# Kernel tuning notes

Measured on AMD Instinct MI355X. Metric: run time of the kernel, lower is better.

Reference implementation:

```python
import jax, jax.numpy as jnp
import numpy as np

C_IN, C_OUT, K, H, W = 16, 16, 3, 1024, 1024
PAD = 1  # 'same' padding for 3x3 stride-1


def setup_inputs() -> dict:
    key = jax.random.key(0)
    kx, kw, kb = jax.random.split(key, 3)
    x = jax.random.normal(kx, (1, C_IN, H, W), dtype=jnp.float32)
    weight = jax.random.normal(kw, (C_OUT, C_IN, K, K), dtype=jnp.float32) * 0.05
    bias = jax.random.normal(kb, (C_OUT,), dtype=jnp.float32) * 0.05
    return {"x": x, "weight": weight, "bias": bias}


def reference(x, weight, bias):
    # Original module: im2col (unfold) + matmul + reshape + bias add.
    # Mathematically identical to a dense 2D convolution (cross-correlation),
    # expressed here as the fused implicit-GEMM conv primitive.
    out = jax.lax.conv_general_dilated(
        x, weight,
        window_strides=(1, 1),
        padding=((PAD, PAD), (PAD, PAD)),
        dimension_numbers=("NCHW", "OIHW", "NCHW"),
    )  # [1, C_OUT, H, W]
    # out_unf.view(*output_shape) drops the batch dim (batch must be 1)
    return out[0] + bias[:, None, None]
```

## Files before the change

kernel.cpp:

```cpp
#include <hip/hip_runtime.h>


#define HH 1024
#define WW 1024
#define CIN 16
#define COUT 16
#define TW 64
#define TH 16
#define LROWS (TH + 2)
#define LCOLS (TW + 2)
#define PIX 16
#define NPIX (LROWS * LCOLS)

typedef short v8s __attribute__((ext_vector_type(8)));
typedef float v4f __attribute__((ext_vector_type(4)));
typedef unsigned int u32;

__device__ __forceinline__ unsigned short f32_bf16(float f) {
    union { float f; u32 u; } v;
    v.f = f;
    u32 u = v.u;
    u += 0x7fffu + ((u >> 16) & 1u);
    return (unsigned short)(u >> 16);
}

__device__ __forceinline__ int swz(int c) { return c ^ ((c >> 3) & 7); }

__global__ __launch_bounds__(256, 3)
void conv3x3_fused(const float* __restrict__ x,
                   const float* __restrict__ wgt,
                   const float* __restrict__ bias,
                   float* __restrict__ out) {
    __shared__ __align__(16) unsigned short sm[NPIX * PIX];
    __shared__ __align__(16) unsigned short wsm[20 * 16 * 8];

    const int tid = threadIdx.x;
    const int lane = tid & 63;
    const int wave = tid >> 6;
    const int h0 = blockIdx.y * TH;
    const int w0 = blockIdx.x * TW;

    if (tid < 32) ((uint4*)(wsm + 18 * 16 * 8))[tid] = make_uint4(0u, 0u, 0u, 0u);
    #pragma unroll
    for (int s = 0; s < 9; ++s) {
        const int e = s * 256 + tid;
        const int m = e / 144;
        const int rem = e - m * 144;
        const int c = rem / 9;
        const int r9 = rem - c * 9;
        const int t = r9 * 2 + (c >> 3);
        wsm[(t * 16 + m) * 8 + (c & 7)] = f32_bf16(wgt[e]);
    }

    auto stage_body = [&](int b) {
        const int r = b >> 4;
        const int j = b & 15;
        const int gh = h0 - 1 + r;
        const int pbase = r * LCOLS + 1 + 4 * j;
        float4 f4[CIN];
        if ((unsigned)gh < (unsigned)HH) {
            const float4* src = (const float4*)(x + (size_t)gh * WW + w0) + j;
            #pragma unroll
            for (int c = 0; c < CIN; ++c)
                f4[c] = src[(size_t)c * (HH * WW / 4)];
        } else {
            #pragma unroll
            for (int c = 0; c < CIN; ++c)
                f4[c] = make_float4(0.f, 0.f, 0.f, 0.f);
        }
        #pragma unroll
        for (int k = 0; k < 4; ++k) {
            u32 pk[8];
            #pragma unroll
            for (int i = 0; i < 8; ++i) {
                const float lo = ((const float*)&f4[2 * i])[k];
                const float hi = ((const float*)&f4[2 * i + 1])[k];
                pk[i] = (u32)f32_bf16(lo) | ((u32)f32_bf16(hi) << 16);
            }
            #pragma unroll
            for (int half = 0; half < 2; ++half) {
                const int cc = 2 * pbase + 2 * k + half;
                *(uint4*)(sm + swz(cc) * 8) = *(uint4*)&pk[half * 4];
            }
        }
    };
    auto stage_halo = [&](int h) {
        const int r = h >> 1;
        const int side = h & 1;
        const int gh = h0 - 1 + r;
        const int gw = side ? (w0 + 64) : (w0 - 1);
        const int p = r * LCOLS + (side ? 65 : 0);
        float f[CIN];
        if ((unsigned)gh < (unsigned)HH && (unsigned)gw < (unsigned)WW) {
            const float* src = x + (size_t)gh * WW + gw;
            #pragma unroll
            for (int c = 0; c < CIN; ++c) f[c] = src[(size_t)c * (HH * WW)];
        } else {
            #pragma unroll
            for (int c = 0; c < CIN; ++c) f[c] = 0.f;
        }
        u32 pk[8];
        #pragma unroll
        for (int i = 0; i < 8; ++i)
            pk[i] = (u32)f32_bf16(f[2 * i]) | ((u32)f32_bf16(f[2 * i + 1]) << 16);
        #pragma unroll
        for (int half = 0; half < 2; ++half) {
            const int cc = 2 * p + half;
            *(uint4*)(sm + swz(cc) * 8) = *(uint4*)&pk[half * 4];
        }
    };

    stage_body(tid);
    if (tid < 32) stage_body(256 + tid);
    else if (tid < 68) stage_halo(tid - 32);

    const int m = lane & 15;
    const int q = lane >> 4;
    const int colbase = wave * 16 + m;

    int Kofs[5];
    #pragma unroll
    for (int g5 = 0; g5 < 5; ++g5) {
        int t = 4 * g5 + q;
        int tt = t > 17 ? 17 : t;
        int khkw = tt >> 1;
        int kh = khkw / 3;
        int kw = khkw - 3 * kh;
        int half = tt & 1;
        Kofs[g5] = (kh * LCOLS + colbase + kw) * 2 + half;
    }
    float bl[4];
    #pragma unroll
    for (int i = 0; i < 4; ++i) bl[i] = bias[q * 4 + i];

    __syncthreads();

    v8s a[5];
    #pragma unroll
    for (int g5 = 0; g5 < 5; ++g5) {
        const int t = 4 * g5 + q;
        a[g5] = *(const v8s*)(wsm + (t * 16 + m) * 8);
    }

    #pragma unroll 4
    for (int r = 0; r < TH; ++r) {
        v4f acc = {0.f, 0.f, 0.f, 0.f};
        #pragma unroll
        for (int g5 = 0; g5 < 5; ++g5) {
            int c = r * (LCOLS * 2) + Kofs[g5];
            v8s b = *(const v8s*)(sm + swz(c) * 8);
            acc = __builtin_amdgcn_mfma_f32_16x16x32_bf16(a[g5], b, acc, 0, 0, 0);
        }
        float* op = out + (size_t)(h0 + r) * WW + (w0 + colbase);
        #pragma unroll
        for (int i = 0; i < 4; ++i)
            op[(size_t)(q * 4 + i) * (HH * WW)] = acc[i] + bl[i];
    }
}

extern "C" void kernel_launch(void* const* d_in, const int* in_sizes, int n_in,
                              void* d_out, int out_size, void* d_ws, size_t ws_size,
                              hipStream_t stream) {
    const float* x = (const float*)d_in[0];
    const float* w = (const float*)d_in[1];
    const float* b = (const float*)d_in[2];
    float* out = (float*)d_out;
    dim3 grid(WW / TW, HH / TH);
    conv3x3_fused<<<grid, dim3(256), 0, stream>>>(x, w, b, out);
}
```

Measured before the change: 128.9 us.

## Switch to single-wave blocks with smaller tiles and register-staged loads

Replaces the 256-thread block with a 64-thread single-wave block that processes an 8x64 tile. Each wave stages its input rows through registers in chunks into LDS, and removes the block barrier. Weights are converted directly from global memory into MFMA operand registers instead of through shared memory. Hardware packed bf16 conversion replaces the software rounding. This trades higher halo overhead and register pressure for more independent blocks and no cross-wave synchronisation.

```diff
diff --git a/kernel.cpp b/kernel.cpp
--- a/kernel.cpp
+++ b/kernel.cpp
@@ -4,121 +4,61 @@
 #define HH 1024
 #define WW 1024
 #define CIN 16
-#define COUT 16
+#define HWP (HH * WW)
 #define TW 64
-#define TH 16
-#define LROWS (TH + 2)
-#define LCOLS (TW + 2)
-#define PIX 16
+#define TH 8
+#define LROWS 10
+#define LCOLS 66
 #define NPIX (LROWS * LCOLS)
 
 typedef short v8s __attribute__((ext_vector_type(8)));
 typedef float v4f __attribute__((ext_vector_type(4)));
 typedef unsigned int u32;
 
-__device__ __forceinline__ unsigned short f32_bf16(float f) {
-    union { float f; u32 u; } v;
-    v.f = f;
-    u32 u = v.u;
-    u += 0x7fffu + ((u >> 16) & 1u);
-    return (unsigned short)(u >> 16);
+__device__ __forceinline__ u32 cvt_pk_bf16(float lo, float hi) {
+    u32 r;
+    asm("v_cvt_pk_bf16_f32 %0, %1, %2" : "=v"(r) : "v"(lo), "v"(hi));
+    return r;
 }
 
 __device__ __forceinline__ int swz(int c) { return c ^ ((c >> 3) & 7); }
 
-__global__ __launch_bounds__(256, 3)
-void conv3x3_fused(const float* __restrict__ x,
-                   const float* __restrict__ wgt,
-                   const float* __restrict__ bias,
-                   float* __restrict__ out) {
-    __shared__ __align__(16) unsigned short sm[NPIX * PIX];
-    __shared__ __align__(16) unsigned short wsm[20 * 16 * 8];
+__global__ __launch_bounds__(64, 2)
+void conv3x3_wave(const float* __restrict__ x,
+                  const float* __restrict__ wgt,
+                  const float* __restrict__ bias,
+                  float* __restrict__ out) {
+    __shared__ __align__(16) unsigned short sm[NPIX * 16];
 
-    const int tid = threadIdx.x;
-    const int lane = tid & 63;
-    const int wave = tid >> 6;
-    const int h0 = blockIdx.y * TH;
-    const int w0 = blockIdx.x * TW;
-
-    if (tid < 32) ((uint4*)(wsm + 18 * 16 * 8))[tid] = make_uint4(0u, 0u, 0u, 0u);
-    #pragma unroll
-    for (int s = 0; s < 9; ++s) {
-        const int e = s * 256 + tid;
-        const int m = e / 144;
-        const int rem = e - m * 144;
-        const int c = rem / 9;
-        const int r9 = rem - c * 9;
-        const int t = r9 * 2 + (c >> 3);
-        wsm[(t * 16 + m) * 8 + (c & 7)] = f32_bf16(wgt[e]);
-    }
-
-    auto stage_body = [&](int b) {
-        const int r = b >> 4;
-        const int j = b & 15;
-        const int gh = h0 - 1 + r;
-        const int pbase = r * LCOLS + 1 + 4 * j;
-        float4 f4[CIN];
-        if ((unsigned)gh < (unsigned)HH) {
-            const float4* src = (const float4*)(x + (size_t)gh * WW + w0) + j;
-            #pragma unroll
-            for (int c = 0; c < CIN; ++c)
-                f4[c] = src[(size_t)c * (HH * WW / 4)];
-        } else {
-            #pragma unroll
-            for (int c = 0; c < CIN; ++c)
-                f4[c] = make_float4(0.f, 0.f, 0.f, 0.f);
-        }
-        #pragma unroll
-        for (int k = 0; k < 4; ++k) {
-            u32 pk[8];
-            #pragma unroll
-            for (int i = 0; i < 8; ++i) {
-                const float lo = ((const float*)&f4[2 * i])[k];
-                const float hi = ((const float*)&f4[2 * i + 1])[k];
-                pk[i] = (u32)f32_bf16(lo) | ((u32)f32_bf16(hi) << 16);
-            }
-            #pragma unroll
-            for (int half = 0; half < 2; ++half) {
-                const int cc = 2 * pbase + 2 * k + half;
-                *(uint4*)(sm + swz(cc) * 8) = *(uint4*)&pk[half * 4];
-            }
-        }
-    };
-    auto stage_halo = [&](int h) {
-        const int r = h >> 1;
-        const int side = h & 1;
-        const int gh = h0 - 1 + r;
-        const int gw = side ? (w0 + 64) : (w0 - 1);
-        const int p = r * LCOLS + (side ? 65 : 0);
-        float f[CIN];
-        if ((unsigned)gh < (unsigned)HH && (unsigned)gw < (unsigned)WW) {
-            const float* src = x + (size_t)gh * WW + gw;
-            #pragma unroll
-            for (int c = 0; c < CIN; ++c) f[c] = src[(size_t)c * (HH * WW)];
-        } else {
-            #pragma unroll
-            for (int c = 0; c < CIN; ++c) f[c] = 0.f;
-        }
-        u32 pk[8];
-        #pragma unroll
-        for (int i = 0; i < 8; ++i)
-            pk[i] = (u32)f32_bf16(f[2 * i]) | ((u32)f32_bf16(f[2 * i + 1]) << 16);
-        #pragma unroll
-        for (int half = 0; half < 2; ++half) {
-            const int cc = 2 * p + half;
-            *(uint4*)(sm + swz(cc) * 8) = *(uint4*)&pk[half * 4];
-        }
-    };
-
-    stage_body(tid);
-    if (tid < 32) stage_body(256 + tid);
-    else if (tid < 68) stage_halo(tid - 32);
-
+    const int lane = threadIdx.x;
     const int m = lane & 15;
     const int q = lane >> 4;
-    const int colbase = wave * 16 + m;
+    const int w0 = blockIdx.x * TW;
+    const int h0 = blockIdx.y * TH;
 
-    int Kofs[5];
+    v8s a[5];
+    #pragma unroll
+    for (int g5 = 0; g5 < 5; ++g5) {
+        const int t = 4 * g5 + q;
+        union { u32 u[4]; v8s v; } wv;
+        if (t < 18) {
+            const int base = m * 144 + (t & 1) * 72 + (t >> 1);
+            #pragma unroll
+            for (int jj = 0; jj < 4; ++jj) {
+                const float lo = wgt[base + 18 * jj];
+                const float hi = wgt[base + 18 * jj + 9];
+                wv.u[jj] = cvt_pk_bf16(lo, hi);
+            }
+        } else {
+            wv.u[0] = wv.u[1] = wv.u[2] = wv.u[3] = 0u;
+        }
+        a[g5] = wv.v;
+    }
+    float bl[4];
+    #pragma unroll
+    for (int i = 0; i < 4; ++i) bl[i] = bias[q * 4 + i];
+
+    int Kbase[5];
     #pragma unroll
     for (int g5 = 0; g5 < 5; ++g5) {
         int t = 4 * g5 + q;
@@ -126,36 +66,114 @@
         int khkw = tt >> 1;
         int kh = khkw / 3;
         int kw = khkw - 3 * kh;
-        int half = tt & 1;
-        Kofs[g5] = (kh * LCOLS + colbase + kw) * 2 + half;
-    }
-    float bl[4];
-    #pragma unroll
-    for (int i = 0; i < 4; ++i) bl[i] = bias[q * 4 + i];
-
-    __syncthreads();
-
-    v8s a[5];
-    #pragma unroll
-    for (int g5 = 0; g5 < 5; ++g5) {
-        const int t = 4 * g5 + q;
-        a[g5] = *(const v8s*)(wsm + (t * 16 + m) * 8);
+        Kbase[g5] = (kh * LCOLS + m + kw) * 2 + (tt & 1);
     }
 
-    #pragma unroll 4
-    for (int r = 0; r < TH; ++r) {
-        v4f acc = {0.f, 0.f, 0.f, 0.f};
+    auto load_body = [&](int s0, int NR, float4* f4) {
+        const int rr = lane >> 4;
+        if (rr < NR) {
+            const int gh = h0 - 1 + s0 + rr;
+            const int j = lane & 15;
+            if ((unsigned)gh < (unsigned)HH) {
+                const float4* src = (const float4*)(x + (size_t)gh * WW + w0) + j;
+                #pragma unroll
+                for (int c = 0; c < CIN; ++c)
+                    f4[c] = src[(size_t)c * (HWP / 4)];
+            } else {
+                #pragma unroll
+                for (int c = 0; c < CIN; ++c)
+                    f4[c] = make_float4(0.f, 0.f, 0.f, 0.f);
+            }
+        }
+    };
+    auto load_halo = [&](int s0, int NR, int lane0, float* f) {
+        const int h = lane - lane0;
+        if ((unsigned)h < (unsigned)(2 * NR)) {
+            const int gh = h0 - 1 + s0 + (h >> 1);
+            const int gw = (h & 1) ? (w0 + TW) : (w0 - 1);
+            if ((unsigned)gh < (unsigned)HH && (unsigned)gw < (unsigned)WW) {
+                const float* src = x + (size_t)gh * WW + gw;
+                #pragma unroll
+                for (int c = 0; c < CIN; ++c) f[c] = src[(size_t)c * HWP];
+            } else {
+                #pragma unroll
+                for (int c = 0; c < CIN; ++c) f[c] = 0.f;
+            }
+        }
+    };
+    auto write_body = [&](int s0, int NR, const float4* f4) {
+        const int rr = lane >> 4;
+        if (rr < NR) {
+            const int slot = s0 + rr;
+            const int j = lane & 15;
+            const int pbase = slot * LCOLS + 1 + 4 * j;
+            #pragma unroll
+            for (int k = 0; k < 4; ++k) {
+                u32 pk[8];
+                #pragma unroll
+                for (int i = 0; i < 8; ++i) {
+                    const float lo = ((const float*)&f4[2 * i])[k];
+                    const float hi = ((const float*)&f4[2 * i + 1])[k];
+                    pk[i] = cvt_pk_bf16(lo, hi);
+                }
+                #pragma unroll
+                for (int half = 0; half < 2; ++half) {
+                    const int cc = 2 * pbase + 2 * k + half;
+                    *(uint4*)(sm + swz(cc) * 8) = *(uint4*)&pk[half * 4];
+                }
+            }
+        }
+    };
+    auto write_halo = [&](int s0, int NR, int lane0, const float* f) {
+        const int h = lane - lane0;
+        if ((unsigned)h < (unsigned)(2 * NR)) {
+            const int slot = s0 + (h >> 1);
+            const int p = slot * LCOLS + ((h & 1) ? 65 : 0);
+            u32 pk[8];
+            #pragma unroll
+            for (int i = 0; i < 8; ++i)
+                pk[i] = cvt_pk_bf16(f[2 * i], f[2 * i + 1]);
+            #pragma unroll
+            for (int half = 0; half < 2; ++half) {
+                const int cc = 2 * p + half;
+                *(uint4*)(sm + swz(cc) * 8) = *(uint4*)&pk[half * 4];
+            }
+        }
+    };
+
+    auto compute4 = [&](int r0) {
         #pragma unroll
-        for (int g5 = 0; g5 < 5; ++g5) {
-            int c = r * (LCOLS * 2) + Kofs[g5];
-            v8s b = *(const v8s*)(sm + swz(c) * 8);
-            acc = __builtin_amdgcn_mfma_f32_16x16x32_bf16(a[g5], b, acc, 0, 0, 0);
+        for (int rr = 0; rr < 4; ++rr) {
+            const int r = r0 + rr;
+            #pragma unroll
+            for (int g16 = 0; g16 < 4; ++g16) {
+                v4f acc = {0.f, 0.f, 0.f, 0.f};
+                #pragma unroll
+                for (int g5 = 0; g5 < 5; ++g5) {
+                    const int c = r * (LCOLS * 2) + g16 * 32 + Kbase[g5];
+                    v8s b = *(const v8s*)(sm + swz(c) * 8);
+                    acc = __builtin_amdgcn_mfma_f32_16x16x32_bf16(a[g5], b, acc, 0, 0, 0);
+                }
+                float* op = out + (size_t)(h0 + r) * WW + (w0 + g16 * 16 + m);
+                #pragma unroll
+                for (int i = 0; i < 4; ++i)
+                    op[(size_t)(q * 4 + i) * HWP] = acc[i] + bl[i];
+            }
         }
-        float* op = out + (size_t)(h0 + r) * WW + (w0 + colbase);
-        #pragma unroll
-        for (int i = 0; i < 4; ++i)
-            op[(size_t)(q * 4 + i) * (HH * WW)] = acc[i] + bl[i];
-    }
+    };
+
+    float4 fA[CIN];
+    float4 fB[CIN];
+    float hA[CIN], hB[CIN], hC[CIN];
+
+    load_body(0, 4, fA);  load_halo(0, 4, 0, hA);
+    load_body(4, 4, fB);  load_halo(4, 4, 0, hB);
+    write_body(0, 4, fA); write_halo(0, 4, 0, hA);
+    load_body(8, 2, fA);  load_halo(8, 2, 32, hC);
+    write_body(4, 4, fB); write_halo(4, 4, 0, hB);
+    write_body(8, 2, fA); write_halo(8, 2, 32, hC);
+    compute4(0);
+    compute4(4);
 }
 
 extern "C" void kernel_launch(void* const* d_in, const int* in_sizes, int n_in,
@@ -166,5 +184,5 @@
     const float* b = (const float*)d_in[2];
     float* out = (float*)d_out;
     dim3 grid(WW / TW, HH / TH);
-    conv3x3_fused<<<grid, dim3(256), 0, stream>>>(x, w, b, out);
+    conv3x3_wave<<<grid, dim3(64), 0, stream>>>(x, w, b, out);
 }
```

Result: slower. 139.8 us (+8.5%).
